# Kernel optimization log

Hardware: AMD Instinct MI355X
Metric: run time of the kernel (lower is better)

Reference implementation:

```python
import jax, jax.numpy as jnp
import numpy as np

S, B, I, H, MLP, K = 1024, 64, 512, 256, 512, 64  # seq_len, batch, input, hidden, mlp, n_sections


def setup_inputs() -> dict:
    key = jax.random.key(0)
    ks = jax.random.split(key, 12)
    inputs = jax.random.normal(ks[0], (S, B, I), jnp.float32)
    input_length = jnp.full((B,), S, dtype=jnp.int32)  # full-length seqs -> pack/pad is identity
    # contiguous section boundaries per document; indices address pad_output of length S+1
    bounds = jnp.sort(jax.random.randint(ks[1], (B, K + 1), 0, S + 1), axis=1)
    begin = bounds[:, :-1].astype(jnp.int32)
    end = bounds[:, 1:].astype(jnp.int32)
    # one-hot section membership per token: [B, S, K]
    sec = jax.random.randint(ks[2], (B, S), 0, K)
    section_indicator = jax.nn.one_hot(sec, K, dtype=jnp.float32)
    s = 1.0 / np.sqrt(H)
    u = lambda k, shape: jax.random.uniform(k, shape, jnp.float32, -s, s)
    params = {
        'W_ih_f': u(ks[3], (3 * H, I)), 'W_hh_f': u(ks[4], (3 * H, H)),
        'b_ih_f': u(ks[5], (3 * H,)), 'b_hh_f': u(ks[5], (3 * H,)),
        'W_ih_b': u(ks[6], (3 * H, I)), 'W_hh_b': u(ks[7], (3 * H, H)),
        'b_ih_b': u(ks[8], (3 * H,)), 'b_hh_b': u(ks[8], (3 * H,)),
        'W1': u(ks[9], (MLP, 4 * H)), 'b1': u(ks[9], (MLP,)),
        'W2': u(ks[10], (1, MLP)), 'b2': u(ks[10], (1,)),
    }
    return dict(inputs=inputs, input_length=input_length,
                section_indicator=section_indicator, begin=begin, end=end, **params)


def _gru_dir(x, Wi, Wh, bi, bh, reverse):
    """One direction of a torch-style GRU. x: [S,B,I] -> hiddens [S,B,H]."""
    xi = jnp.einsum('sbi,gi->sbg', x, Wi) + bi  # precompute input projections [S,B,3H]
    Bsz = x.shape[1]
    Hn = Wh.shape[1]

    def step(h, xt):
        gh = h @ Wh.T + bh
        xr, xz, xn = jnp.split(xt, 3, axis=-1)
        hr, hz, hn = jnp.split(gh, 3, axis=-1)
        r = jax.nn.sigmoid(xr + hr)
        z = jax.nn.sigmoid(xz + hz)
        n = jnp.tanh(xn + r * hn)
        hnew = (1.0 - z) * n + z * h
        return hnew, hnew

    h0 = jnp.zeros((Bsz, Hn), x.dtype)
    _, hs = jax.lax.scan(step, h0, xi, reverse=reverse)
    return hs


def reference(inputs, input_length, section_indicator, begin, end,
              W_ih_f, W_hh_f, b_ih_f, b_hh_f,
              W_ih_b, W_hh_b, b_ih_b, b_hh_b,
              W1, b1, W2, b2):
    # bi-GRU (dropout layers are identity in eval mode)
    out_f = _gru_dir(inputs, W_ih_f, W_hh_f, b_ih_f, b_hh_f, reverse=False)
    out_b = _gru_dir(inputs, W_ih_b, W_hh_b, b_ih_b, b_hh_b, reverse=True)
    output = jnp.concatenate([out_f, out_b], axis=-1)  # [S,B,2H]
    # prepend zero row along time: pad_output [S+1,B,2H]
    pad_output = jnp.concatenate([jnp.zeros((1,) + output.shape[1:], output.dtype), output], axis=0)
    po = jnp.transpose(pad_output, (1, 0, 2))  # [B,S+1,2H]
    g_end = jnp.take_along_axis(po, end[:, :, None], axis=1)    # [B,K,2H]
    g_beg = jnp.take_along_axis(po, begin[:, :, None], axis=1)  # [B,K,2H]
    Hn = output.shape[-1] // 2
    local = jnp.concatenate([g_end[..., :Hn] - g_beg[..., :Hn],
                             g_beg[..., Hn:] - g_end[..., Hn:]], axis=-1)  # [B,K,2H]
    lcr = jnp.einsum('bsk,bkd->bsd', section_indicator, local)  # [B,S,2H]
    lcr = jnp.transpose(lcr, (1, 0, 2))  # [S,B,2H]
    mlp_in = jnp.concatenate([output, lcr], axis=-1)  # [S,B,4H]
    h1 = jax.nn.relu(mlp_in @ W1.T + b1)
    out = h1 @ W2.T + b2  # [S,B,1]
    return out
```

## Files before the change

kernel.cpp:

```cpp
#include <hip/hip_runtime.h>

typedef unsigned short u16;
typedef __attribute__((ext_vector_type(2))) unsigned short u16x2;
typedef __attribute__((ext_vector_type(8))) short short8;
typedef __attribute__((ext_vector_type(4))) float f32x4;
typedef __attribute__((ext_vector_type(4))) int i32x4;

#define T_CHUNK 128
#define XI_DIRSZ ((size_t)T_CHUNK * 49152)

__device__ __forceinline__ u16 f2bf(float f) {
  unsigned u = __float_as_uint(f);
  u += 0x7FFFu + ((u >> 16) & 1u);
  return (u16)(u >> 16);
}
__device__ __forceinline__ float bf2f(u16 v) { return __uint_as_float(((unsigned)v) << 16); }
__device__ __forceinline__ short8 cvt8(const float* __restrict__ p) {
  float4 a = ((const float4*)p)[0];
  float4 b = ((const float4*)p)[1];
  short8 r;
  r[0] = (short)f2bf(a.x); r[1] = (short)f2bf(a.y); r[2] = (short)f2bf(a.z); r[3] = (short)f2bf(a.w);
  r[4] = (short)f2bf(b.x); r[5] = (short)f2bf(b.y); r[6] = (short)f2bf(b.z); r[7] = (short)f2bf(b.w);
  return r;
}

__global__ __launch_bounds__(256) void k_diag(float* o, float v) {
  if (threadIdx.x == 0 && blockIdx.x == 0) o[0] = v;
}

__global__ __launch_bounds__(256) void k_cvt(const float* __restrict__ s, u16* __restrict__ d, int n) {
  int i = blockIdx.x * 256 + threadIdx.x;
  int st = gridDim.x * 256;
  for (; i < n; i += st) d[i] = f2bf(s[i]);
}

__global__ __launch_bounds__(64) void k_quantw(const float* __restrict__ Wf, const float* __restrict__ Wb,
                                               signed char* __restrict__ Wq, float* __restrict__ rscale) {
  const int row = blockIdx.x;
  const int l = threadIdx.x;
  const float* src = (row < 768) ? (Wf + (size_t)row * 256) : (Wb + (size_t)(row - 768) * 256);
  float4 v = ((const float4*)src)[l];
  float m = fmaxf(fmaxf(fabsf(v.x), fabsf(v.y)), fmaxf(fabsf(v.z), fabsf(v.w)));
#pragma unroll
  for (int off = 32; off; off >>= 1) m = fmaxf(m, __shfl_xor(m, off));
  const float s = 127.f / m;
  char4 q;
  q.x = (signed char)(int)__builtin_rintf(v.x * s);
  q.y = (signed char)(int)__builtin_rintf(v.y * s);
  q.z = (signed char)(int)__builtin_rintf(v.z * s);
  q.w = (signed char)(int)__builtin_rintf(v.w * s);
  ((char4*)(Wq + (size_t)row * 256))[l] = q;
  if (l == 0) rscale[row] = m / (127.f * 127.f);
}

__device__ __forceinline__ int swz8b(int row, int off) {
  return row * 256 + ((((off >> 4) ^ (row * 5)) & 15) << 4) + (off & 15);
}

__global__ __launch_bounds__(512, 1) void k_fused(
    const float* __restrict__ x, const u16* __restrict__ WihB,
    const float* __restrict__ bihf, const float* __restrict__ bihb,
    u16* __restrict__ xi, const signed char* __restrict__ Wq, const float* __restrict__ rscale,
    const float* __restrict__ bhhf, const float* __restrict__ bhhb,
    float* __restrict__ carry, u16* __restrict__ ob, int chunk, int nscan) {
  __shared__ __align__(16) signed char hb8[2][1024];
  __shared__ __align__(16) u16 Al[64 * 72];
  __shared__ __align__(16) u16 Bl[64 * 72];
  __shared__ char pad_[65536];

  const int tid = threadIdx.x;
  const int l = tid & 63, w = tid >> 6;
  const int lm = l & 15, lq = l >> 4;
  if (nscan == -2) pad_[tid] = (char)chunk;

  if ((int)blockIdx.x >= nscan) {
    const int cn = chunk + 1;
    const int pid = blockIdx.x - nscan;
    const int dir = pid >= 1536;
    const int q = dir ? pid - 1536 : pid;
    const int r8 = q & 7, rest = q >> 3;
    const int bx = rest % 12;
    const int by = (rest / 12) * 8 + r8;
    const float* A = x + ((size_t)(dir ? (1024 - (cn + 1) * T_CHUNK) : (cn * T_CHUNK)) + by) * 32768;
    const u16* Bw = WihB + (size_t)dir * 393216;
    const float* bias = dir ? bihb : bihf;
    u16* xo = xi + ((size_t)((cn & 1) * 2 + dir)) * XI_DIRSZ;

    const int n0 = bx << 6;
    const int r0 = tid >> 3, c0 = (tid & 7) << 3;
    const int mt = w >> 1, nh = w & 1;
    f32x4 acc[2] = {};
    for (int k0 = 0; k0 < 512; k0 += 64) {
      __syncthreads();
      *(short8*)&Al[r0 * 72 + c0] = cvt8(A + (size_t)r0 * 512 + k0 + c0);
      *(short8*)&Bl[r0 * 72 + c0] = *(const short8*)(Bw + (size_t)(n0 + r0) * 512 + k0 + c0);
      __syncthreads();
#pragma unroll
      for (int kk = 0; kk < 2; ++kk) {
        short8 af = *(const short8*)&Al[(mt * 16 + lm) * 72 + kk * 32 + lq * 8];
#pragma unroll
        for (int ntp = 0; ntp < 2; ++ntp) {
          short8 bf = *(const short8*)&Bl[((nh * 2 + ntp) * 16 + lm) * 72 + kk * 32 + lq * 8];
          acc[ntp] = __builtin_amdgcn_mfma_f32_16x16x32_bf16(af, bf, acc[ntp], 0, 0, 0);
        }
      }
    }
#pragma unroll
    for (int ntp = 0; ntp < 2; ++ntp) {
      int n = n0 + (nh * 2 + ntp) * 16 + lm;
      float bv = bias[n];
#pragma unroll
      for (int r = 0; r < 4; ++r) {
        int b = mt * 16 + lq * 4 + r;
        xo[(((size_t)by * 8 + (b >> 3)) * 768 + n) * 8 + (b & 7)] = f2bf(acc[ntp][r] + bv);
      }
    }
    return;
  }

  __builtin_amdgcn_s_setprio(1);
  const int dir = blockIdx.x >> 4;
  const int grp = blockIdx.x & 15;
  const int jhL = lq >> 1;
  const int b0 = (lq & 1) << 1;
  const int jL = w * 32 + jhL * 16 + lm;
  const int arow = lm & 3;
  const float* bhh = dir ? bhhb : bhhf;
  const u16* xic = xi + ((size_t)((chunk & 1) * 2 + dir)) * XI_DIRSZ;

  i32x4 bw[6][4];
#pragma unroll
  for (int g = 0; g < 3; ++g)
#pragma unroll
    for (int jh = 0; jh < 2; ++jh) {
      const int row = dir * 768 + g * 256 + w * 32 + jh * 16 + lm;
      const signed char* rp = Wq + (size_t)row * 256 + lq * 16;
#pragma unroll
      for (int kk = 0; kk < 4; ++kk) bw[g * 2 + jh][kk] = *(const i32x4*)(rp + kk * 64);
    }
  float rs[3];
#pragma unroll
  for (int g = 0; g < 3; ++g) rs[g] = rscale[dir * 768 + g * 256 + jL];
  const float bR = bhh[jL], bZ = bhh[256 + jL], bN = bhh[512 + jL];

  signed char* hbb = &hb8[0][0];
  float hreg[2];
  if (chunk == 0) {
    hreg[0] = 0.f; hreg[1] = 0.f;
    if (tid < 512) ((unsigned*)hbb)[tid] = 0;
  } else {
#pragma unroll
    for (int i = 0; i < 2; ++i) {
      float v = carry[(size_t)(dir * 64 + grp * 4 + b0 + i) * 256 + jL];
      hreg[i] = v;
      hbb[swz8b(b0 + i, jL)] = (signed char)(int)__builtin_rintf(fminf(fmaxf(v, -1.f), 1.f) * 127.f);
    }
  }

  const int stL0 = dir ? (T_CHUNK - 1) : 0;
  const u16* p_xi = xic + ((size_t)stL0 * 8 + (grp >> 1)) * 6144 + (size_t)jL * 8 + (grp & 1) * 4 + b0;
  const int tg0 = dir ? (1023 - chunk * T_CHUNK) : (chunk * T_CHUNK);
  u16* p_ob = ob + ((size_t)(tg0 * 64 + grp * 4 + b0)) * 512 + dir * 256 + jL;
  const ptrdiff_t dxi = dir ? -49152 : 49152;
  const ptrdiff_t dob = dir ? -32768 : 32768;
  __syncthreads();

  u16x2 xv[3];
#pragma unroll
  for (int g = 0; g < 3; ++g) xv[g] = *(const u16x2*)(p_xi + g * 2048);

  for (int st = 0; st < T_CHUNK; ++st) {
    const int cur = st & 1;
    const signed char* hcur = hbb + cur * 1024;
    i32x4 a4[4];
#pragma unroll
    for (int kk = 0; kk < 4; ++kk) a4[kk] = *(const i32x4*)(hcur + swz8b(arow, kk * 64 + lq * 16));
    p_xi += dxi;
    u16x2 xn[3];
    if (st < T_CHUNK - 1) {
#pragma unroll
      for (int g = 0; g < 3; ++g) xn[g] = *(const u16x2*)(p_xi + g * 2048);
    }

    i32x4 acc[2][3] = {};
#pragma unroll
    for (int kk = 0; kk < 4; ++kk)
#pragma unroll
      for (int jh = 0; jh < 2; ++jh)
#pragma unroll
        for (int g = 0; g < 3; ++g)
          acc[jh][g] = __builtin_amdgcn_mfma_i32_16x16x64_i8(a4[kk], bw[g * 2 + jh][kk], acc[jh][g], 0, 0, 0);

    signed char* hnxt = hbb + (cur ^ 1) * 1024;
    i32x4 accS[3];
#pragma unroll
    for (int g = 0; g < 3; ++g) accS[g] = (lq >= 2) ? acc[1][g] : acc[0][g];
#pragma unroll
    for (int i = 0; i < 2; ++i) {
      float fr = (float)((lq & 1) ? accS[0][2 + i] : accS[0][i]) * rs[0];
      float fz = (float)((lq & 1) ? accS[1][2 + i] : accS[1][i]) * rs[1];
      float fn = (float)((lq & 1) ? accS[2][2 + i] : accS[2][i]) * rs[2];
      float ar = bf2f(xv[0][i]) + fr + bR;
      float az = bf2f(xv[1][i]) + fz + bZ;
      float rr = __builtin_amdgcn_rcpf(1.f + __expf(-ar));
      float zz = __builtin_amdgcn_rcpf(1.f + __expf(-az));
      float an = bf2f(xv[2][i]) + rr * (fn + bN);
      float nn = 2.f * __builtin_amdgcn_rcpf(1.f + __expf(-2.f * an)) - 1.f;
      float hv = nn + zz * (hreg[i] - nn);
      hreg[i] = hv;
      hnxt[swz8b(b0 + i, jL)] = (signed char)(int)__builtin_rintf(fminf(fmaxf(hv, -1.f), 1.f) * 127.f);
      p_ob[(size_t)i * 512] = f2bf(hv);
    }
#pragma unroll
    for (int g = 0; g < 3; ++g) xv[g] = xn[g];
    p_ob += dob;
    asm volatile("s_waitcnt lgkmcnt(0)\n\ts_barrier" ::: "memory");
  }
  __builtin_amdgcn_s_setprio(0);
#pragma unroll
  for (int i = 0; i < 2; ++i)
    carry[(size_t)(dir * 64 + grp * 4 + b0 + i) * 256 + jL] = hreg[i];
}

__global__ __launch_bounds__(256) void k_local(const u16* __restrict__ ob, const int* __restrict__ bg,
                                               const int* __restrict__ en, u16* __restrict__ loc) {
  const int b = blockIdx.y, k = blockIdx.x, j = threadIdx.x;
  const int e = en[b * 64 + k], g = bg[b * 64 + k];
  const float ef  = e ? bf2f(ob[(size_t)((e - 1) * 64 + b) * 512 + j]) : 0.f;
  const float bf_ = g ? bf2f(ob[(size_t)((g - 1) * 64 + b) * 512 + j]) : 0.f;
  const float eb  = e ? bf2f(ob[(size_t)((e - 1) * 64 + b) * 512 + 256 + j]) : 0.f;
  const float bb_ = g ? bf2f(ob[(size_t)((g - 1) * 64 + b) * 512 + 256 + j]) : 0.f;
  const size_t o = ((size_t)b * 64 + k) * 512;
  loc[o + j] = f2bf(ef - bf_);
  loc[o + 256 + j] = f2bf(bb_ - eb);
}

__global__ __launch_bounds__(256) void k_sec(const float* __restrict__ ind, int* __restrict__ sec) {
  const int idx = blockIdx.x * 256 + threadIdx.x;
  const int s = idx >> 6, b = idx & 63;
  const float* row = ind + ((size_t)b * 1024 + s) * 64;
  int kk = 0;
  for (int q = 0; q < 64; ++q)
    if (row[q] > 0.5f) kk = q;
  sec[idx] = kk;
}

__global__ __launch_bounds__(256) void k_gemm_mlp(const u16* __restrict__ obb, const u16* __restrict__ locb,
                                                  const int* __restrict__ sec, const u16* __restrict__ W1b,
                                                  const float* __restrict__ b1, const float* __restrict__ W2,
                                                  float* __restrict__ partial) {
  __shared__ __align__(16) u16 Al[64 * 72];
  __shared__ __align__(16) u16 Bl[64 * 72];
  const int tid = threadIdx.x;
  const int l = tid & 63, w = tid >> 6;
  const int lm = l & 15, lq = l >> 4;
  const int flat = blockIdx.x + blockIdx.y * 8;
  const int xcd = flat & 7, idx = flat >> 3;
  const int bxs = idx & 7;
  const int bys = xcd * 128 + (idx >> 3);
  const int m0 = bys << 6, n0 = bxs << 6;
  const int r0 = tid >> 3, c0 = (tid & 7) << 3;
  const int mA = m0 + r0, mB = mA + 32;
  const u16* pa0 = obb + (size_t)mA * 512;
  const u16* pa1 = obb + (size_t)mB * 512;
  const u16* la0 = locb + ((size_t)(mA & 63) * 64 + sec[mA]) * 512 - 512;
  const u16* la1 = locb + ((size_t)(mB & 63) * 64 + sec[mB]) * 512 - 512;
  f32x4 acc[4] = {};
  for (int k0 = 0; k0 < 1024; k0 += 64) {
    __syncthreads();
    const u16* sa0 = (k0 < 512) ? pa0 : la0;
    const u16* sa1 = (k0 < 512) ? pa1 : la1;
    *(short8*)&Al[r0 * 72 + c0]        = *(const short8*)(sa0 + k0 + c0);
    *(short8*)&Al[(r0 + 32) * 72 + c0] = *(const short8*)(sa1 + k0 + c0);
    *(short8*)&Bl[r0 * 72 + c0]        = *(const short8*)(W1b + (size_t)(n0 + r0) * 1024 + k0 + c0);
    *(short8*)&Bl[(r0 + 32) * 72 + c0] = *(const short8*)(W1b + (size_t)(n0 + r0 + 32) * 1024 + k0 + c0);
    __syncthreads();
#pragma unroll
    for (int kk = 0; kk < 2; ++kk) {
      short8 af = *(const short8*)&Al[(w * 16 + lm) * 72 + kk * 32 + lq * 8];
#pragma unroll
      for (int nt = 0; nt < 4; ++nt) {
        short8 bf = *(const short8*)&Bl[(nt * 16 + lm) * 72 + kk * 32 + lq * 8];
        acc[nt] = __builtin_amdgcn_mfma_f32_16x16x32_bf16(af, bf, acc[nt], 0, 0, 0);
      }
    }
  }
  float s[4] = {0.f, 0.f, 0.f, 0.f};
#pragma unroll
  for (int nt = 0; nt < 4; ++nt) {
    int n = n0 + nt * 16 + lm;
    float bb = b1[n], ww = W2[n];
#pragma unroll
    for (int r = 0; r < 4; ++r) s[r] += fmaxf(acc[nt][r] + bb, 0.f) * ww;
  }
#pragma unroll
  for (int off = 1; off < 16; off <<= 1)
#pragma unroll
    for (int r = 0; r < 4; ++r) s[r] += __shfl_xor(s[r], off);
  if (lm == 0) {
#pragma unroll
    for (int r = 0; r < 4; ++r)
      partial[(size_t)bxs * 65536 + m0 + w * 16 + lq * 4 + r] = s[r];
  }
}

__global__ __launch_bounds__(256) void k_fin2(const float* __restrict__ partial, const float* __restrict__ b2,
                                              float* __restrict__ o) {
  const int i = blockIdx.x * 256 + threadIdx.x;
  float s = b2[0];
#pragma unroll
  for (int q = 0; q < 8; ++q) s += partial[(size_t)q * 65536 + i];
  o[i] = s;
}

extern "C" void kernel_launch(void* const* d_in, const int* in_sizes, int n_in,
                              void* d_out, int out_size, void* d_ws, size_t ws_size,
                              hipStream_t stream) {
  (void)in_sizes; (void)n_in; (void)out_size;
  const float* x    = (const float*)d_in[0];
  const float* sind = (const float*)d_in[2];
  const int*   beg  = (const int*)d_in[3];
  const int*   endi = (const int*)d_in[4];
  const float* Wihf = (const float*)d_in[5];
  const float* Whhf = (const float*)d_in[6];
  const float* bihf = (const float*)d_in[7];
  const float* bhhf = (const float*)d_in[8];
  const float* Wihb = (const float*)d_in[9];
  const float* Whhb = (const float*)d_in[10];
  const float* bihb = (const float*)d_in[11];
  const float* bhhb = (const float*)d_in[12];
  const float* W1   = (const float*)d_in[13];
  const float* b1   = (const float*)d_in[14];
  const float* W2   = (const float*)d_in[15];
  const float* b2   = (const float*)d_in[16];

  const size_t NEED = 124911616ull;
  if (ws_size < NEED) {
    k_diag<<<dim3(1), dim3(256), 0, stream>>>((float*)d_out, 1000.f + (float)(ws_size >> 20));
    return;
  }

  char* ws = (char*)d_ws;
  u16*   xibuf = (u16*)(ws);
  u16*   obb   = (u16*)(ws + 50331648);
  u16*   locb  = (u16*)(ws + 117440512);
  int*   sec   = (int*)(ws + 121634816);
  float* part  = (float*)(ws + 121896960);
  signed char* Wq = (signed char*)(ws + 123994112);
  float* rscale = (float*)(ws + 124387328);
  float* carry = (float*)(ws + 124780544);
  u16*   WihB  = (u16*)(ws + 117440512);
  u16*   W1b   = (u16*)(ws);

  k_quantw<<<dim3(1536), dim3(64), 0, stream>>>(Whhf, Whhb, Wq, rscale);
  k_cvt<<<dim3(128), dim3(256), 0, stream>>>(Wihf, WihB, 393216);
  k_cvt<<<dim3(128), dim3(256), 0, stream>>>(Wihb, WihB + 393216, 393216);

  k_fused<<<dim3(3072), dim3(512), 0, stream>>>(x, WihB, bihf, bihb, xibuf, Wq, rscale,
                                                bhhf, bhhb, carry, obb, -1, 0);
  for (int c = 0; c < 8; ++c)
    k_fused<<<dim3(c < 7 ? 3104 : 32), dim3(512), 0, stream>>>(x, WihB, bihf, bihb, xibuf, Wq, rscale,
                                                               bhhf, bhhb, carry, obb, c, 32);

  k_cvt<<<dim3(256), dim3(256), 0, stream>>>(W1, W1b, 524288);
  k_local<<<dim3(64, 64), dim3(256), 0, stream>>>(obb, beg, endi, locb);
  k_sec<<<dim3(256), dim3(256), 0, stream>>>(sind, sec);
  k_gemm_mlp<<<dim3(8, 1024), dim3(256), 0, stream>>>(obb, locb, sec, W1b, b1, W2, part);
  k_fin2<<<dim3(256), dim3(256), 0, stream>>>(part, b2, (float*)d_out);
}
```

Baseline: 1.048 ms.

## Retile MLP GEMM to 256x64 blocks with register-prefetched A and swizzled LDS B

The MLP GEMM block tile grows from 64x64 to 256x64, with each wave computing 64 rows across four M sub-tiles so every B fragment feeds four MFMAs. A fragments are now loaded straight from global memory into registers and prefetched one K-step ahead, which removes the A shared-memory staging. B is staged through an XOR-swizzled LDS tile in place of padding, and its next tile is also prefetched into registers. This cuts LDS traffic and W1 reloads, but register pressure rises (64 accumulators plus prefetch buffers), the grid drops to 2048 blocks, and the XCD-aware block remapping is gone.

```diff
diff --git a/kernel.cpp b/kernel.cpp
--- a/kernel.cpp
+++ b/kernel.cpp
@@ -249,58 +249,93 @@
                                                   const int* __restrict__ sec, const u16* __restrict__ W1b,
                                                   const float* __restrict__ b1, const float* __restrict__ W2,
                                                   float* __restrict__ partial) {
-  __shared__ __align__(16) u16 Al[64 * 72];
-  __shared__ __align__(16) u16 Bl[64 * 72];
+  __shared__ __align__(16) u16 Bl[64][64];
   const int tid = threadIdx.x;
   const int l = tid & 63, w = tid >> 6;
   const int lm = l & 15, lq = l >> 4;
-  const int flat = blockIdx.x + blockIdx.y * 8;
-  const int xcd = flat & 7, idx = flat >> 3;
-  const int bxs = idx & 7;
-  const int bys = xcd * 128 + (idx >> 3);
-  const int m0 = bys << 6, n0 = bxs << 6;
-  const int r0 = tid >> 3, c0 = (tid & 7) << 3;
-  const int mA = m0 + r0, mB = mA + 32;
-  const u16* pa0 = obb + (size_t)mA * 512;
-  const u16* pa1 = obb + (size_t)mB * 512;
-  const u16* la0 = locb + ((size_t)(mA & 63) * 64 + sec[mA]) * 512 - 512;
-  const u16* la1 = locb + ((size_t)(mB & 63) * 64 + sec[mB]) * 512 - 512;
-  f32x4 acc[4] = {};
+  const int mb = blockIdx.x >> 3, nh = blockIdx.x & 7;
+  const int m0 = mb << 8, n0 = nh << 6;
+
+  const u16* pa[4];
+  const u16* la[4];
+#pragma unroll
+  for (int mt = 0; mt < 4; ++mt) {
+    int mA = m0 + w * 64 + mt * 16 + lm;
+    pa[mt] = obb + (size_t)mA * 512;
+    la[mt] = locb + ((size_t)(mA & 63) * 64 + sec[mA]) * 512 - 512;
+  }
+  const int br = tid >> 2;
+  const int bc = (tid & 3) << 4;
+  const int ch0 = (tid & 3) << 1;
+  const u16* wrow = W1b + (size_t)(n0 + br) * 1024 + bc;
+
+  short8 rb0 = *(const short8*)(wrow);
+  short8 rb1 = *(const short8*)(wrow + 8);
+  short8 rA[4][2];
+#pragma unroll
+  for (int mt = 0; mt < 4; ++mt)
+#pragma unroll
+    for (int kk = 0; kk < 2; ++kk) rA[mt][kk] = *(const short8*)(pa[mt] + kk * 32 + lq * 8);
+
+  f32x4 acc[4][4] = {};
   for (int k0 = 0; k0 < 1024; k0 += 64) {
     __syncthreads();
-    const u16* sa0 = (k0 < 512) ? pa0 : la0;
-    const u16* sa1 = (k0 < 512) ? pa1 : la1;
-    *(short8*)&Al[r0 * 72 + c0]        = *(const short8*)(sa0 + k0 + c0);
-    *(short8*)&Al[(r0 + 32) * 72 + c0] = *(const short8*)(sa1 + k0 + c0);
-    *(short8*)&Bl[r0 * 72 + c0]        = *(const short8*)(W1b + (size_t)(n0 + r0) * 1024 + k0 + c0);
-    *(short8*)&Bl[(r0 + 32) * 72 + c0] = *(const short8*)(W1b + (size_t)(n0 + r0 + 32) * 1024 + k0 + c0);
+    *(short8*)&Bl[br][((ch0 ^ (br & 7)) << 3)] = rb0;
+    *(short8*)&Bl[br][(((ch0 | 1) ^ (br & 7)) << 3)] = rb1;
     __syncthreads();
-#pragma unroll
-    for (int kk = 0; kk < 2; ++kk) {
-      short8 af = *(const short8*)&Al[(w * 16 + lm) * 72 + kk * 32 + lq * 8];
+    short8 aCur[4][2];
+#pragma unroll
+    for (int mt = 0; mt < 4; ++mt)
+#pragma unroll
+      for (int kk = 0; kk < 2; ++kk) aCur[mt][kk] = rA[mt][kk];
+    if (k0 < 960) {
+      const int kn = k0 + 64;
+      rb0 = *(const short8*)(wrow + kn);
+      rb1 = *(const short8*)(wrow + kn + 8);
+#pragma unroll
+      for (int mt = 0; mt < 4; ++mt) {
+        const u16* base = (kn < 512) ? pa[mt] : la[mt];
+#pragma unroll
+        for (int kk = 0; kk < 2; ++kk) rA[mt][kk] = *(const short8*)(base + kn + kk * 32 + lq * 8);
+      }
+    }
+#pragma unroll
+    for (int kk = 0; kk < 2; ++kk)
 #pragma unroll
       for (int nt = 0; nt < 4; ++nt) {
-        short8 bf = *(const short8*)&Bl[(nt * 16 + lm) * 72 + kk * 32 + lq * 8];
-        acc[nt] = __builtin_amdgcn_mfma_f32_16x16x32_bf16(af, bf, acc[nt], 0, 0, 0);
+        const int rrow = nt * 16 + lm;
+        short8 bf = *(const short8*)&Bl[rrow][(((kk * 4 + lq) ^ (rrow & 7)) << 3)];
+#pragma unroll
+        for (int mt = 0; mt < 4; ++mt)
+          acc[mt][nt] = __builtin_amdgcn_mfma_f32_16x16x32_bf16(aCur[mt][kk], bf, acc[mt][nt], 0, 0, 0);
       }
-    }
-  }
-  float s[4] = {0.f, 0.f, 0.f, 0.f};
+  }
+  float s[4][4];
+#pragma unroll
+  for (int mt = 0; mt < 4; ++mt)
+#pragma unroll
+    for (int r = 0; r < 4; ++r) s[mt][r] = 0.f;
 #pragma unroll
   for (int nt = 0; nt < 4; ++nt) {
     int n = n0 + nt * 16 + lm;
     float bb = b1[n], ww = W2[n];
 #pragma unroll
-    for (int r = 0; r < 4; ++r) s[r] += fmaxf(acc[nt][r] + bb, 0.f) * ww;
+    for (int mt = 0; mt < 4; ++mt)
+#pragma unroll
+      for (int r = 0; r < 4; ++r) s[mt][r] += fmaxf(acc[mt][nt][r] + bb, 0.f) * ww;
   }
 #pragma unroll
   for (int off = 1; off < 16; off <<= 1)
 #pragma unroll
-    for (int r = 0; r < 4; ++r) s[r] += __shfl_xor(s[r], off);
+    for (int mt = 0; mt < 4; ++mt)
+#pragma unroll
+      for (int r = 0; r < 4; ++r) s[mt][r] += __shfl_xor(s[mt][r], off);
   if (lm == 0) {
 #pragma unroll
-    for (int r = 0; r < 4; ++r)
-      partial[(size_t)bxs * 65536 + m0 + w * 16 + lq * 4 + r] = s[r];
+    for (int mt = 0; mt < 4; ++mt)
+#pragma unroll
+      for (int r = 0; r < 4; ++r)
+        partial[(size_t)nh * 65536 + m0 + w * 64 + mt * 16 + lq * 4 + r] = s[mt][r];
   }
 }
 
@@ -365,6 +400,6 @@
   k_cvt<<<dim3(256), dim3(256), 0, stream>>>(W1, W1b, 524288);
   k_local<<<dim3(64, 64), dim3(256), 0, stream>>>(obb, beg, endi, locb);
   k_sec<<<dim3(256), dim3(256), 0, stream>>>(sind, sec);
-  k_gemm_mlp<<<dim3(8, 1024), dim3(256), 0, stream>>>(obb, locb, sec, W1b, b1, W2, part);
+  k_gemm_mlp<<<dim3(2048), dim3(256), 0, stream>>>(obb, locb, sec, W1b, b1, W2, part);
   k_fin2<<<dim3(256), dim3(256), 0, stream>>>(part, b2, (float*)d_out);
 }
```

After: 1.059 ms. No clear change (+1.0%).
